# Performance work log

Hardware: AMD Instinct MI355X
Metric: run time of the kernel (lower is better)

Reference implementation:

```python
import jax, jax.numpy as jnp
import numpy as np

B, N, E, C, M = 4, 16384, 65536, 256, 64

def setup_inputs() -> dict:
    key = jax.random.key(0)
    ks = jax.random.split(key, 12)
    s = 1.0 / np.sqrt(C)
    return {
        'x': jax.random.normal(ks[0], (B, N, C), jnp.float32),
        'edge_attr': jax.random.normal(ks[1], (B, E, 1), jnp.float32),
        'edge_idx': jax.random.randint(ks[2], (B, E, 2), 0, N, jnp.int32),
        'W_fx': jax.random.normal(ks[3], (C, C), jnp.float32) * s,
        'b_fx': jnp.zeros((C,), jnp.float32),
        'W_x': jax.random.normal(ks[4], (C, C), jnp.float32) * s,
        'b_x': jnp.zeros((C,), jnp.float32),
        'W_slice': jax.random.normal(ks[5], (C, M), jnp.float32) * s,
        'b_slice': jnp.zeros((M,), jnp.float32),
        'temp_x': jnp.full((1, 1, M), 0.5, jnp.float32),
        'ph_x': jax.random.uniform(ks[6], (1, 1, C), jnp.float32) / C,
        'W_fedge': jax.random.normal(ks[7], (1, C), jnp.float32),
        'b_fedge': jnp.zeros((C,), jnp.float32),
        'temp_edge': jnp.full((1, 1, M), 0.5, jnp.float32),
        'W_eslice': jax.random.normal(ks[8], (M, M), jnp.float32) * (1.0 / np.sqrt(M)),
        'b_eslice': jnp.zeros((M,), jnp.float32),
        'ph_edge': jax.random.uniform(ks[9], (1, 1, C), jnp.float32) / C,
    }


def reference(x, edge_attr, edge_idx, W_fx, b_fx, W_x, b_x, W_slice, b_slice,
              temp_x, ph_x, W_fedge, b_fedge, temp_edge, W_eslice, b_eslice, ph_edge):
    # node path
    fx_mid = x @ W_fx + b_fx                                  # [B,N,C]
    x_mid = x @ W_x + b_x + ph_x                              # [B,N,C]
    logits = (x_mid @ W_slice + b_slice) / jnp.clip(temp_x, 0.01, 5.0)
    slice_weight = jax.nn.softmax(logits, axis=-1)            # [B,N,M]
    slice_norm = slice_weight.sum(axis=-2)[..., None]         # [B,M,1]
    slice_token = jnp.einsum('bnm,bnc->bmc', slice_weight, fx_mid)
    # edge path
    fedge_mid = edge_attr @ W_fedge + b_fedge + ph_edge       # [B,E,C]
    gather = jax.vmap(lambda sw, idx: sw[idx])                # per-batch node gather
    sw_sum = gather(slice_weight, edge_idx[:, :, 0]) + gather(slice_weight, edge_idx[:, :, 1])
    e_logits = (sw_sum / jnp.clip(temp_edge, 0.01, 5.0)) @ W_eslice + b_eslice
    edge_slice_weight = jax.nn.softmax(e_logits, axis=-1)     # [B,E,M]
    edge_slice_norm = edge_slice_weight.sum(axis=-2)[..., None]
    edge_slice_token = jnp.einsum('bnm,bnc->bmc', edge_slice_weight, fedge_mid)
    scale = x.shape[1] / edge_attr.shape[1]
    slice_token = slice_token + edge_slice_token * scale
    slice_norm = slice_norm + edge_slice_norm * scale
    slice_token = slice_token / (slice_norm + 1e-5)
    return (slice_token, slice_weight)
```

## Files before the change

kernel.cpp:

```cpp
#include <hip/hip_runtime.h>

#define BB 4
#define NN 16384
#define EE 65536
#define CC 256
#define MM 64

#define WS_NORM   0
#define WS_T1     256
#define WS_ESN    512
#define WS_BCOMB  768
#define WS_ITX    832
#define WS_ITE    896
#define WS_WES2   1024
#define WS_WCOMB  5120
#define WS_WES2T  13312
#define WS_SW2    21504
#define WS_SSUM   WS_SW2
#define WS_SPART  4215808

typedef __attribute__((ext_vector_type(8))) __bf16 bf16x8_t;
typedef __attribute__((ext_vector_type(4))) float f32x4_t;

static __device__ __forceinline__ unsigned short f2bf(float f) {
    unsigned int u = __float_as_uint(f);
    unsigned int r = (u + 0x7FFFu + ((u >> 16) & 1u)) >> 16;
    return (unsigned short)r;
}

__global__ __launch_bounds__(256) void kPP(const float* __restrict__ Wx,
                                           const float* __restrict__ Wsl,
                                           const float* __restrict__ bx,
                                           const float* __restrict__ phx,
                                           const float* __restrict__ bsl,
                                           const float* __restrict__ tx,
                                           const float* __restrict__ te,
                                           const float* __restrict__ Wes,
                                           float* __restrict__ ws) {
    __shared__ float row[256];
    __shared__ float part[4][64];
    const int tid = threadIdx.x;
    const int m = tid & 63, kq = tid >> 6;
    if (blockIdx.x < 256) {
        const int c = blockIdx.x;
        row[tid] = Wx[c * CC + tid];
        __syncthreads();
        float acc = 0.f;
#pragma unroll 8
        for (int kk = 0; kk < 64; ++kk) {
            int k = kq * 64 + kk;
            acc += row[k] * Wsl[k * MM + m];
        }
        part[kq][m] = acc;
        __syncthreads();
        if (tid < 64) {
            float v = part[0][tid] + part[1][tid] + part[2][tid] + part[3][tid];
            ((unsigned short*)(ws + WS_WCOMB))[tid * 256 + c] = f2bf(v);
        }
    } else {
#pragma unroll
        for (int i = 0; i < 3; ++i) ws[i * 256 + tid] = 0.f;
        row[tid] = bx[tid] + phx[tid];
        __syncthreads();
        float acc = 0.f;
#pragma unroll 8
        for (int kk = 0; kk < 64; ++kk) {
            int k = kq * 64 + kk;
            acc += row[k] * Wsl[k * MM + m];
        }
        part[kq][m] = acc;
        __syncthreads();
        if (tid < 64) {
            ws[WS_BCOMB + tid] = bsl[tid] +
                part[0][tid] + part[1][tid] + part[2][tid] + part[3][tid];
            ws[WS_ITX + tid] = 1.f / fminf(fmaxf(tx[tid], 0.01f), 5.f);
            ws[WS_ITE + tid] = 1.f / fminf(fmaxf(te[tid], 0.01f), 5.f);
        }
        unsigned short* w2t = (unsigned short*)(ws + WS_WES2T);
#pragma unroll
        for (int i = 0; i < 16; ++i) {
            int e = i * 256 + tid;
            int m2 = e >> 6, k2 = e & 63;
            float itk = 1.f / fminf(fmaxf(te[k2], 0.01f), 5.f);
            w2t[m2 * 64 + k2] = f2bf(itk * Wes[k2 * 64 + m2]);
        }
    }
}

__global__ __launch_bounds__(256, 2) void kN1(const float* __restrict__ x,
                                              const float* __restrict__ ws,
                                              float* __restrict__ out1,
                                              unsigned short* __restrict__ sw2b,
                                              float* __restrict__ norm_acc) {
    __shared__ float smem[17920];
    __shared__ float redn[4][64];
    __shared__ float bcs[64], itxs[64];
    unsigned short* smem_u = (unsigned short*)smem;
    float* swl = smem + 4096;
    const int tid = threadIdx.x;
    const int wv = tid >> 6, l = tid & 63;
    const int ln = l & 15, kg = l >> 4;
    const int row0 = blockIdx.x * 128;
    const int b = blockIdx.x >> 7;
    const int r = tid >> 2;
    const int h = tid & 3;

    if (tid < 64) { bcs[tid] = ws[WS_BCOMB + tid]; itxs[tid] = ws[WS_ITX + tid]; }

    const unsigned short* wct = (const unsigned short*)(ws + WS_WCOMB);
#pragma unroll
    for (int i = 0; i < 8; ++i) {
        int f8 = (i * 256 + tid) * 8;
        int m = f8 >> 8, k = f8 & 255;
        *(uint4*)&smem_u[m * 264 + k] = *(const uint4*)&wct[f8];
    }
    __syncthreads();

    f32x4_t acc[2][4];
#pragma unroll
    for (int i = 0; i < 2; ++i)
#pragma unroll
        for (int j = 0; j < 4; ++j) acc[i][j] = (f32x4_t){0.f, 0.f, 0.f, 0.f};

    for (int c0 = 0; c0 < CC; c0 += 32) {
        bf16x8_t bf[4];
#pragma unroll
        for (int mt = 0; mt < 4; ++mt)
            bf[mt] = *(const bf16x8_t*)&smem_u[(mt * 16 + ln) * 264 + c0 + kg * 8];
#pragma unroll
        for (int rt = 0; rt < 2; ++rt) {
            int arow = row0 + (wv * 2 + rt) * 16 + ln;
            const float* ap = x + (size_t)arow * CC + c0 + kg * 8;
            float4 p0 = *(const float4*)ap;
            float4 p1 = *(const float4*)(ap + 4);
            union { unsigned short u[8]; bf16x8_t v; } af;
            af.u[0] = f2bf(p0.x); af.u[1] = f2bf(p0.y);
            af.u[2] = f2bf(p0.z); af.u[3] = f2bf(p0.w);
            af.u[4] = f2bf(p1.x); af.u[5] = f2bf(p1.y);
            af.u[6] = f2bf(p1.z); af.u[7] = f2bf(p1.w);
#pragma unroll
            for (int mt = 0; mt < 4; ++mt)
                acc[rt][mt] = __builtin_amdgcn_mfma_f32_16x16x32_bf16(
                    af.v, bf[mt], acc[rt][mt], 0, 0, 0);
        }
    }
    __syncthreads();

#pragma unroll
    for (int rt = 0; rt < 2; ++rt)
#pragma unroll
        for (int mt = 0; mt < 4; ++mt)
#pragma unroll
            for (int j = 0; j < 4; ++j)
                swl[((wv * 2 + rt) * 16 + kg * 4 + j) * 68 + mt * 16 + ln] =
                    acc[rt][mt][j];
    {
        const unsigned short* w2tg = (const unsigned short*)(ws + WS_WES2T);
        int m2 = tid >> 2, k2 = (tid & 3) * 16;
        *(uint4*)&smem_u[m2 * 80 + k2] = *(const uint4*)&w2tg[m2 * 64 + k2];
        *(uint4*)&smem_u[m2 * 80 + k2 + 8] = *(const uint4*)&w2tg[m2 * 64 + k2 + 8];
    }
    __syncthreads();

    float sacc[2][16];
#pragma unroll
    for (int i = 0; i < 2; ++i)
#pragma unroll
        for (int q = 0; q < 4; ++q) {
            float4 v = *(float4*)&swl[(r + 64 * i) * 68 + h * 16 + q * 4];
            sacc[i][q * 4 + 0] = v.x; sacc[i][q * 4 + 1] = v.y;
            sacc[i][q * 4 + 2] = v.z; sacc[i][q * 4 + 3] = v.w;
        }
    float colsum[16];
#pragma unroll
    for (int j = 0; j < 16; ++j) colsum[j] = 0.f;
#pragma unroll
    for (int i = 0; i < 2; ++i) {
        float mx = -1e30f;
#pragma unroll
        for (int j = 0; j < 16; ++j) {
            int m = h * 16 + j;
            sacc[i][j] = (sacc[i][j] + bcs[m]) * itxs[m];
            mx = fmaxf(mx, sacc[i][j]);
        }
        mx = fmaxf(mx, __shfl_xor(mx, 1));
        mx = fmaxf(mx, __shfl_xor(mx, 2));
        float s = 0.f;
#pragma unroll
        for (int j = 0; j < 16; ++j) { sacc[i][j] = __expf(sacc[i][j] - mx); s += sacc[i][j]; }
        s += __shfl_xor(s, 1);
        s += __shfl_xor(s, 2);
        float inv = 1.f / s;
        int rl = r + 64 * i;
        int row = row0 + rl;
#pragma unroll
        for (int q = 0; q < 4; ++q) {
            float4 v = {sacc[i][q * 4 + 0] * inv, sacc[i][q * 4 + 1] * inv,
                        sacc[i][q * 4 + 2] * inv, sacc[i][q * 4 + 3] * inv};
            *(float4*)(out1 + (size_t)row * MM + h * 16 + q * 4) = v;
            *(float4*)&swl[rl * 68 + h * 16 + q * 4] = v;
#pragma unroll
            for (int j = 0; j < 4; ++j) colsum[q * 4 + j] += ((float*)&v)[j];
        }
    }
#pragma unroll
    for (int j = 0; j < 16; ++j) {
        colsum[j] += __shfl_xor(colsum[j], 4);
        colsum[j] += __shfl_xor(colsum[j], 8);
        colsum[j] += __shfl_xor(colsum[j], 16);
        colsum[j] += __shfl_xor(colsum[j], 32);
    }
    if (l < 4) {
#pragma unroll
        for (int j = 0; j < 16; ++j) redn[wv][h * 16 + j] = colsum[j];
    }
    __syncthreads();

    f32x4_t eacc[2][4];
#pragma unroll
    for (int i = 0; i < 2; ++i)
#pragma unroll
        for (int j = 0; j < 4; ++j) eacc[i][j] = (f32x4_t){0.f, 0.f, 0.f, 0.f};
#pragma unroll
    for (int ks = 0; ks < 2; ++ks) {
        bf16x8_t bfw[4];
#pragma unroll
        for (int mt = 0; mt < 4; ++mt)
            bfw[mt] = *(const bf16x8_t*)&smem_u[(mt * 16 + ln) * 80 + ks * 32 + kg * 8];
#pragma unroll
        for (int rt = 0; rt < 2; ++rt) {
            const float* ap = &swl[((wv * 2 + rt) * 16 + ln) * 68 + ks * 32 + kg * 8];
            float4 p0 = *(const float4*)ap;
            float4 p1 = *(const float4*)(ap + 4);
            union { unsigned short u[8]; bf16x8_t v; } af;
            af.u[0] = f2bf(p0.x); af.u[1] = f2bf(p0.y);
            af.u[2] = f2bf(p0.z); af.u[3] = f2bf(p0.w);
            af.u[4] = f2bf(p1.x); af.u[5] = f2bf(p1.y);
            af.u[6] = f2bf(p1.z); af.u[7] = f2bf(p1.w);
#pragma unroll
            for (int mt = 0; mt < 4; ++mt)
                eacc[rt][mt] = __builtin_amdgcn_mfma_f32_16x16x32_bf16(
                    af.v, bfw[mt], eacc[rt][mt], 0, 0, 0);
        }
    }
    {
        unsigned short* esb = (unsigned short*)(smem + 12800);
#pragma unroll
        for (int rt = 0; rt < 2; ++rt)
#pragma unroll
            for (int mt = 0; mt < 4; ++mt)
#pragma unroll
                for (int j = 0; j < 4; ++j)
                    esb[((wv * 2 + rt) * 16 + kg * 4 + j) * 80 + mt * 16 + ln] =
                        f2bf(eacc[rt][mt][j]);
    }
    __syncthreads();
    {
        const unsigned short* esb = (const unsigned short*)(smem + 12800);
        int row = tid >> 1, half = tid & 1;
        const uint4* src = (const uint4*)&esb[row * 80 + half * 32];
        uint4* dst = (uint4*)(sw2b + (size_t)(row0 + row) * MM + half * 32);
        dst[0] = src[0]; dst[1] = src[1]; dst[2] = src[2]; dst[3] = src[3];
    }

    if (tid < 64)
        atomicAdd(&norm_acc[b * MM + tid],
                  redn[0][tid] + redn[1][tid] + redn[2][tid] + redn[3][tid]);
}

__global__ __launch_bounds__(256, 4) void kEN2(const float* __restrict__ x,
                                               const float* __restrict__ sw,
                                               float* __restrict__ Spart,
                                               int PB, int rowsPB, int nb2,
                                               const float* __restrict__ eattr,
                                               const int* __restrict__ eidx,
                                               const unsigned short* __restrict__ sw2b,
                                               const float* __restrict__ bes,
                                               float* __restrict__ t1_acc,
                                               float* __restrict__ esn_acc) {
    __shared__ float smem[9280];
    const int tid = threadIdx.x;
    if ((int)blockIdx.x < nb2) {
        unsigned short* xT = (unsigned short*)smem;
        unsigned short* sT = (unsigned short*)(smem + 2560);
        const int bid = blockIdx.x;
        const int ch = bid & 1;
        const int p = (bid >> 1) % PB, b = (bid >> 1) / PB;
        const int base = b * NN + p * rowsPB;
        const int wv = tid >> 6, l = tid & 63;
        const int ln = l & 15, kg = l >> 4;
        const int ct0 = wv * 2;

        f32x4_t acc[2][4];
#pragma unroll
        for (int i = 0; i < 2; ++i)
#pragma unroll
            for (int j = 0; j < 4; ++j) acc[i][j] = (f32x4_t){0.f, 0.f, 0.f, 0.f};

        for (int r0 = 0; r0 < rowsPB; r0 += 32) {
            __syncthreads();
#pragma unroll
            for (int i = 0; i < 4; ++i) {
                int flat = i * 256 + tid;
                int rr = flat >> 5, c = (flat & 31) * 4;
                float4 v = *(const float4*)(x + (size_t)(base + r0 + rr) * CC + ch * 128 + c);
                int key = (c >> 2) & 3;
                int off = ((rr >> 3) ^ key) * 8 + (rr & 7);
                xT[(c + 0) * 40 + off] = f2bf(v.x);
                xT[(c + 1) * 40 + off] = f2bf(v.y);
                xT[(c + 2) * 40 + off] = f2bf(v.z);
                xT[(c + 3) * 40 + off] = f2bf(v.w);
            }
#pragma unroll
            for (int i = 0; i < 2; ++i) {
                int flat = i * 256 + tid;
                int rr = flat >> 4, m = (flat & 15) * 4;
                float4 v = *(const float4*)(sw + (size_t)(base + r0 + rr) * MM + m);
                int key = (m >> 2) & 3;
                int off = ((rr >> 3) ^ key) * 8 + (rr & 7);
                sT[(m + 0) * 40 + off] = f2bf(v.x);
                sT[(m + 1) * 40 + off] = f2bf(v.y);
                sT[(m + 2) * 40 + off] = f2bf(v.z);
                sT[(m + 3) * 40 + off] = f2bf(v.w);
            }
            __syncthreads();
            bf16x8_t afr[4];
#pragma unroll
            for (int mt = 0; mt < 4; ++mt) {
                int m = mt * 16 + ln;
                int chunk = kg ^ ((m >> 2) & 3);
                afr[mt] = *(const bf16x8_t*)&sT[m * 40 + chunk * 8];
            }
#pragma unroll
            for (int ct = 0; ct < 2; ++ct) {
                int c = (ct0 + ct) * 16 + ln;
                int chunk = kg ^ ((c >> 2) & 3);
                bf16x8_t bfr = *(const bf16x8_t*)&xT[c * 40 + chunk * 8];
#pragma unroll
                for (int mt = 0; mt < 4; ++mt)
                    acc[ct][mt] = __builtin_amdgcn_mfma_f32_16x16x32_bf16(
                        afr[mt], bfr, acc[ct][mt], 0, 0, 0);
            }
        }
        float* dst = Spart + (size_t)(b * PB + p) * MM * CC + ch * 128;
#pragma unroll
        for (int ct = 0; ct < 2; ++ct)
#pragma unroll
            for (int mt = 0; mt < 4; ++mt)
#pragma unroll
                for (int j = 0; j < 4; ++j) {
                    int m = mt * 16 + kg * 4 + j;
                    int c = (ct0 + ct) * 16 + ln;
                    dst[(size_t)m * CC + c] = acc[ct][mt][j];
                }
    } else {
        float* u    = smem;
        float* eav  = smem + 8448;
        float* redt = smem + 8704;
        float* redn = smem + 8960;
        float* bes_s = smem + 9216;
        const int w = tid >> 6, l = tid & 63;
        const int eg = ((int)blockIdx.x - nb2) * 256 + tid;
        const int b = eg >> 16;
        if (tid < 64) bes_s[tid] = bes[tid];
        const int2 idx = ((const int2*)eidx)[eg];
        const float ea = eattr[eg];
        const uint4* g0 = (const uint4*)(sw2b + (size_t)(b * NN + idx.x) * MM);
        const uint4* g1 = (const uint4*)(sw2b + (size_t)(b * NN + idx.y) * MM);
        eav[w * 64 + l] = ea;
        __syncthreads();

        float v[64];
#pragma unroll
        for (int q = 0; q < 8; ++q) {
            uint4 a = g0[q], c = g1[q];
            unsigned int au[4] = {a.x, a.y, a.z, a.w};
            unsigned int cu[4] = {c.x, c.y, c.z, c.w};
#pragma unroll
            for (int j = 0; j < 4; ++j) {
                int m = q * 8 + j * 2;
                v[m + 0] = __uint_as_float(au[j] << 16) + __uint_as_float(cu[j] << 16) + bes_s[m + 0];
                v[m + 1] = __uint_as_float(au[j] & 0xFFFF0000u) + __uint_as_float(cu[j] & 0xFFFF0000u) + bes_s[m + 1];
            }
        }
        float mx = -1e30f;
#pragma unroll
        for (int m = 0; m < 64; ++m) mx = fmaxf(mx, v[m]);
        float s = 0.f;
#pragma unroll
        for (int m = 0; m < 64; ++m) { v[m] = __expf(v[m] - mx); s += v[m]; }
        float inv = 1.f / s;

        const int ml = l & 31, rh = l >> 5;
#pragma unroll
        for (int ph = 0; ph < 2; ++ph) {
            __syncthreads();
#pragma unroll
            for (int j = 0; j < 32; ++j) u[w * 2112 + l * 33 + j] = v[ph * 32 + j] * inv;
            __syncthreads();
            float t = 0.f, n = 0.f;
#pragma unroll 8
            for (int rr = 0; rr < 32; ++rr) {
                int r = rh * 32 + rr;
                float e = u[w * 2112 + r * 33 + ml];
                n += e;
                t += e * eav[w * 64 + r];
            }
            t += __shfl_xor(t, 32);
            n += __shfl_xor(n, 32);
            if (l < 32) { redt[w * 64 + ph * 32 + l] = t; redn[w * 64 + ph * 32 + l] = n; }
        }
        __syncthreads();
        if (tid < 64) {
            atomicAdd(&t1_acc[b * 64 + tid],
                      redt[tid] + redt[64 + tid] + redt[128 + tid] + redt[192 + tid]);
            atomicAdd(&esn_acc[b * 64 + tid],
                      redn[tid] + redn[64 + tid] + redn[128 + tid] + redn[192 + tid]);
        }
    }
}

__global__ __launch_bounds__(256) void kR(const float* __restrict__ Spart,
                                          float* __restrict__ Ssum, int PB) {
    const int idx = blockIdx.x * 256 + threadIdx.x;
    const int b = idx >> 14;
    const int mc = idx & 16383;
    const float* sp = Spart + (size_t)b * PB * MM * CC + mc;
    float a0 = 0.f, a1 = 0.f, a2 = 0.f, a3 = 0.f;
    for (int p = 0; p < PB; p += 4) {
        a0 += sp[(size_t)(p + 0) * MM * CC];
        a1 += sp[(size_t)(p + 1) * MM * CC];
        a2 += sp[(size_t)(p + 2) * MM * CC];
        a3 += sp[(size_t)(p + 3) * MM * CC];
    }
    Ssum[idx] = (a0 + a1) + (a2 + a3);
}

__global__ __launch_bounds__(256) void kF2(const float* __restrict__ ws,
                                           const float* __restrict__ Wfx,
                                           const float* __restrict__ bfx,
                                           const float* __restrict__ Wfe,
                                           const float* __restrict__ bfe,
                                           const float* __restrict__ phe,
                                           float* __restrict__ out0) {
    __shared__ float srow[256];
    const int bid = blockIdx.x;
    const int b = bid >> 6, m = bid & 63;
    const int t = threadIdx.x;
    srow[t] = ws[WS_SSUM + (size_t)(b * MM + m) * CC + t];
    __syncthreads();
    float acc = 0.f;
#pragma unroll 8
    for (int k = 0; k < 256; ++k) acc += srow[k] * Wfx[k * CC + t];
    float nv  = ws[WS_NORM + b * 64 + m];
    float t1v = ws[WS_T1   + b * 64 + m];
    float ev  = ws[WS_ESN  + b * 64 + m];
    const float scale = (float)NN / (float)EE;
    float num = acc + nv * bfx[t] + scale * (t1v * Wfe[t] + ev * (bfe[t] + phe[t]));
    float den = nv + scale * ev + 1e-5f;
    out0[(size_t)(b * MM + m) * CC + t] = num / den;
}

extern "C" void kernel_launch(void* const* d_in, const int* in_sizes, int n_in,
                              void* d_out, int out_size, void* d_ws, size_t ws_size,
                              hipStream_t stream) {
    const float* x     = (const float*)d_in[0];
    const float* eattr = (const float*)d_in[1];
    const int*   eidx  = (const int*)d_in[2];
    const float* Wfx   = (const float*)d_in[3];
    const float* bfx   = (const float*)d_in[4];
    const float* Wx    = (const float*)d_in[5];
    const float* bx    = (const float*)d_in[6];
    const float* Wsl   = (const float*)d_in[7];
    const float* bsl   = (const float*)d_in[8];
    const float* tx    = (const float*)d_in[9];
    const float* phx   = (const float*)d_in[10];
    const float* Wfe   = (const float*)d_in[11];
    const float* bfe   = (const float*)d_in[12];
    const float* te    = (const float*)d_in[13];
    const float* Wes   = (const float*)d_in[14];
    const float* bes   = (const float*)d_in[15];
    const float* phe   = (const float*)d_in[16];

    float* out0 = (float*)d_out;
    float* out1 = out0 + (size_t)BB * MM * CC;
    float* ws   = (float*)d_ws;
    unsigned short* sw2b = (unsigned short*)(ws + WS_SW2);

    int PB = 64;
    while (PB > 8) {
        size_t need = (size_t)(WS_SPART + (size_t)BB * PB * MM * CC) * sizeof(float);
        if (need <= ws_size) break;
        PB >>= 1;
    }
    int rowsPB = NN / PB;
    int nb2 = BB * PB * 2;

    kPP<<<257, 256, 0, stream>>>(Wx, Wsl, bx, phx, bsl, tx, te, Wes, ws);
    kN1<<<512, 256, 0, stream>>>(x, ws, out1, sw2b, ws + WS_NORM);
    kEN2<<<nb2 + EE * BB / 256, 256, 0, stream>>>(x, out1, ws + WS_SPART, PB, rowsPB, nb2,
                                                  eattr, eidx, sw2b, bes,
                                                  ws + WS_T1, ws + WS_ESN);
    kR <<<1024, 256, 0, stream>>>(ws + WS_SPART, ws + WS_SSUM, PB);
    kF2<<<256, 256, 0, stream>>>(ws, Wfx, bfx, Wfe, bfe, phe, out0);
}
```

Measured before the change: 98.01 us.

## Shrink kEN2 shared memory via bf16 edge staging and raise occupancy

The edge branch now stages its softmax weights in shared memory as bf16 instead of fp32, which roughly halves the LDS footprint of kEN2. The launch-bounds occupancy hint rises from 4 to 6 blocks. The node branch now loads two rows per thread and writes packed pairs of bf16 values as 32-bit LDS stores, which cuts the number of shared stores. The aims are more resident waves to hide gather and global-load latency and fewer LDS instructions, at the cost of rounding the edge weights to bf16 and possible register pressure under the tighter bound.

```diff
diff --git a/kernel.cpp b/kernel.cpp
--- a/kernel.cpp
+++ b/kernel.cpp
@@ -26,6 +26,12 @@
     unsigned int u = __float_as_uint(f);
     unsigned int r = (u + 0x7FFFu + ((u >> 16) & 1u)) >> 16;
     return (unsigned short)r;
+}
+static __device__ __forceinline__ float bf2f(unsigned short h) {
+    return __uint_as_float((unsigned int)h << 16);
+}
+static __device__ __forceinline__ unsigned int pk2(float a, float b) {
+    return (unsigned int)f2bf(a) | ((unsigned int)f2bf(b) << 16);
 }
 
 __global__ __launch_bounds__(256) void kPP(const float* __restrict__ Wx,
@@ -268,7 +274,7 @@
                   redn[0][tid] + redn[1][tid] + redn[2][tid] + redn[3][tid]);
 }
 
-__global__ __launch_bounds__(256, 4) void kEN2(const float* __restrict__ x,
+__global__ __launch_bounds__(256, 6) void kEN2(const float* __restrict__ x,
                                                const float* __restrict__ sw,
                                                float* __restrict__ Spart,
                                                int PB, int rowsPB, int nb2,
@@ -278,7 +284,7 @@
                                                const float* __restrict__ bes,
                                                float* __restrict__ t1_acc,
                                                float* __restrict__ esn_acc) {
-    __shared__ float smem[9280];
+    __shared__ float smem[5184];
     const int tid = threadIdx.x;
     if ((int)blockIdx.x < nb2) {
         unsigned short* xT = (unsigned short*)smem;
@@ -300,28 +306,33 @@
         for (int r0 = 0; r0 < rowsPB; r0 += 32) {
             __syncthreads();
 #pragma unroll
-            for (int i = 0; i < 4; ++i) {
-                int flat = i * 256 + tid;
-                int rr = flat >> 5, c = (flat & 31) * 4;
-                float4 v = *(const float4*)(x + (size_t)(base + r0 + rr) * CC + ch * 128 + c);
-                int key = (c >> 2) & 3;
-                int off = ((rr >> 3) ^ key) * 8 + (rr & 7);
-                xT[(c + 0) * 40 + off] = f2bf(v.x);
-                xT[(c + 1) * 40 + off] = f2bf(v.y);
-                xT[(c + 2) * 40 + off] = f2bf(v.z);
-                xT[(c + 3) * 40 + off] = f2bf(v.w);
+            for (int i = 0; i < 2; ++i) {
+                int task = i * 256 + tid;
+                int rp = task >> 5;
+                int cq = (task & 31) * 4;
+                int ra = 2 * rp;
+                const float* xa = x + (size_t)(base + r0 + ra) * CC + ch * 128 + cq;
+                float4 va = *(const float4*)xa;
+                float4 vb = *(const float4*)(xa + CC);
+                int key = (cq >> 2) & 3;
+                int off = ((ra >> 3) ^ key) * 8 + (ra & 7);
+                *(unsigned int*)&xT[(cq + 0) * 40 + off] = pk2(va.x, vb.x);
+                *(unsigned int*)&xT[(cq + 1) * 40 + off] = pk2(va.y, vb.y);
+                *(unsigned int*)&xT[(cq + 2) * 40 + off] = pk2(va.z, vb.z);
+                *(unsigned int*)&xT[(cq + 3) * 40 + off] = pk2(va.w, vb.w);
             }
-#pragma unroll
-            for (int i = 0; i < 2; ++i) {
-                int flat = i * 256 + tid;
-                int rr = flat >> 4, m = (flat & 15) * 4;
-                float4 v = *(const float4*)(sw + (size_t)(base + r0 + rr) * MM + m);
-                int key = (m >> 2) & 3;
-                int off = ((rr >> 3) ^ key) * 8 + (rr & 7);
-                sT[(m + 0) * 40 + off] = f2bf(v.x);
-                sT[(m + 1) * 40 + off] = f2bf(v.y);
-                sT[(m + 2) * 40 + off] = f2bf(v.z);
-                sT[(m + 3) * 40 + off] = f2bf(v.w);
+            {
+                int rp = tid >> 4, mq = (tid & 15) * 4;
+                int ra = 2 * rp;
+                const float* sa = sw + (size_t)(base + r0 + ra) * MM + mq;
+                float4 va = *(const float4*)sa;
+                float4 vb = *(const float4*)(sa + MM);
+                int key = (mq >> 2) & 3;
+                int off = ((ra >> 3) ^ key) * 8 + (ra & 7);
+                *(unsigned int*)&sT[(mq + 0) * 40 + off] = pk2(va.x, vb.x);
+                *(unsigned int*)&sT[(mq + 1) * 40 + off] = pk2(va.y, vb.y);
+                *(unsigned int*)&sT[(mq + 2) * 40 + off] = pk2(va.z, vb.z);
+                *(unsigned int*)&sT[(mq + 3) * 40 + off] = pk2(va.w, vb.w);
             }
             __syncthreads();
             bf16x8_t afr[4];
@@ -354,11 +365,11 @@
                     dst[(size_t)m * CC + c] = acc[ct][mt][j];
                 }
     } else {
-        float* u    = smem;
-        float* eav  = smem + 8448;
-        float* redt = smem + 8704;
-        float* redn = smem + 8960;
-        float* bes_s = smem + 9216;
+        unsigned short* uu = (unsigned short*)smem;
+        float* eav  = smem + 4352;
+        float* redt = smem + 4608;
+        float* redn = smem + 4864;
+        float* bes_s = smem + 5120;
         const int w = tid >> 6, l = tid & 63;
         const int eg = ((int)blockIdx.x - nb2) * 256 + tid;
         const int b = eg >> 16;
@@ -396,13 +407,15 @@
         for (int ph = 0; ph < 2; ++ph) {
             __syncthreads();
 #pragma unroll
-            for (int j = 0; j < 32; ++j) u[w * 2112 + l * 33 + j] = v[ph * 32 + j] * inv;
+            for (int j = 0; j < 32; j += 2)
+                *(unsigned int*)&uu[w * 2176 + l * 34 + j] =
+                    pk2(v[ph * 32 + j] * inv, v[ph * 32 + j + 1] * inv);
             __syncthreads();
             float t = 0.f, n = 0.f;
 #pragma unroll 8
             for (int rr = 0; rr < 32; ++rr) {
                 int r = rh * 32 + rr;
-                float e = u[w * 2112 + r * 33 + ml];
+                float e = bf2f(uu[w * 2176 + r * 34 + ml]);
                 n += e;
                 t += e * eav[w * 64 + r];
             }
```

Result: slower. 113.7 us (+16.0%).
